# Optimization experiments

Hardware: AMD Instinct MI355X
Metric: run time of the kernel (lower is better)

The kernel has to match this reference:

```python
import jax, jax.numpy as jnp
import numpy as np

B, DIN, DOUT = 16, 64, 64
P1_, P2_, P3_ = 64, 32, 16
BN_EPS = 1e-5


def setup_inputs() -> dict:
    key = jax.random.key(0)
    ks = jax.random.split(key, 8)
    A = jax.random.normal(ks[0], (B, DIN, P1_, P2_, P3_), dtype=jnp.float32)
    ini_p = float(np.sqrt(3.0 / DOUT / DIN))
    ini_qk = float(np.sqrt(1.0 / DOUT / DIN))
    def uni(k, s):
        return jax.random.uniform(k, (DOUT, DIN), dtype=jnp.float32, minval=-s, maxval=s)
    return {
        "A": A,
        "P1": uni(ks[1], ini_p),
        "P2": uni(ks[2], ini_p),
        "P3": uni(ks[3], ini_p),
        "P4": uni(ks[4], ini_p),
        "q": uni(ks[5], ini_qk),
        "k": uni(ks[6], ini_qk),
        "gamma": jnp.ones((DOUT,), jnp.float32),
        "beta": jnp.zeros((DOUT,), jnp.float32),
        "permutation_size1": P1_,
        "permutation_size2": P2_,
        "permutation_size3": P3_,
        "BATCH_SIZE": B,
    }


def reference(A, P1, P2, P3, P4, q, k, gamma, beta,
              permutation_size1, permutation_size2, permutation_size3, BATCH_SIZE):
    b = BATCH_SIZE
    dout = P1.shape[0]
    p1, p2, p3 = permutation_size1, permutation_size2, permutation_size3
    # branch 1: full per-element channel mix  [B, dout, p1, p2, p3]
    A1 = jnp.einsum('oi,bixyz->boxyz', P1, A)
    # branch 2: mean over p3, project, broadcast over p3
    A2 = jnp.einsum('oi,bixy->boxy', P2, A.mean(-1))[..., None]
    # branch 3: mean over p2, project, broadcast over p2
    A3 = jnp.einsum('oi,bixz->boxz', P3, A.mean(-2))[:, :, :, None, :]
    # attention over p1 with flattened (p2*p3) as the contraction axis
    Q = jnp.einsum('oi,bixyz->boxyz', q, A).reshape(b, dout, p1, p2 * p3)
    K = jnp.einsum('oi,bixyz->boxyz', k, A).reshape(b, dout, p1, p2 * p3)
    Alpha = jnp.einsum('bcxm,bcym->bcxy', Q, K)  # [B, dout, p1, p1]
    Alpha_norm = jnp.abs(Alpha) / jnp.linalg.norm(Alpha, axis=3, keepdims=True)
    V = jnp.einsum('oi,bixyz->boxyz', P4, A).reshape(b, dout, p1, p2 * p3)
    Y = jnp.einsum('bcxy,bcym->bcxm', Alpha_norm, V).reshape(b, dout, p1, p2, p3)
    out = A1 + 0.1 * A2 + 0.1 * A3 + 0.1 * Y
    out = jax.nn.relu(out)
    # BatchNorm3d (training-mode batch statistics, biased variance)
    mean = out.mean(axis=(0, 2, 3, 4), keepdims=True)
    var = out.var(axis=(0, 2, 3, 4), keepdims=True)
    out = (out - mean) * jax.lax.rsqrt(var + BN_EPS)
    out = out * gamma[None, :, None, None, None] + beta[None, :, None, None, None]
    return out
```

## Files before the change

kernel.cpp:

```cpp
#include <hip/hip_runtime.h>

typedef __attribute__((ext_vector_type(8))) short short8;
typedef __attribute__((ext_vector_type(4))) float f32x4;
typedef __attribute__((ext_vector_type(8))) unsigned short u16x8;
typedef __attribute__((ext_vector_type(4))) unsigned short u16x4;
typedef __attribute__((ext_vector_type(4))) unsigned int u32x4;
typedef unsigned short u16;

#define DEVINL __device__ __forceinline__

DEVINL u16 f2bf(float f) {
  unsigned u = __builtin_bit_cast(unsigned, f);
  unsigned r = (u + 0x7fffu + ((u >> 16) & 1u)) >> 16;
  return (u16)r;
}
DEVINL float bf2f(u16 h) {
  unsigned u = ((unsigned)h) << 16;
  return __builtin_bit_cast(float, u);
}
DEVINL unsigned pk2(float a, float b) {
  return (unsigned)f2bf(a) | ((unsigned)f2bf(b) << 16);
}
DEVINL int swzc(int row, int chunk) { return chunk ^ ((row ^ (row >> 3)) & 7); }
DEVINL int tile_byte(int row, int chunk) { return row * 128 + swzc(row, chunk) * 16; }


__global__ void kw_convert(const float* __restrict__ P1, const float* __restrict__ q,
                           const float* __restrict__ k, const float* __restrict__ P4,
                           const float* __restrict__ P2, const float* __restrict__ P3,
                           u16* __restrict__ Wbf) {
  int t = threadIdx.x;
  const float* srcs[6] = {P1, q, k, P4, P2, P3};
  for (int w = 0; w < 6; ++w)
    for (int e = t; e < 4096; e += 256) Wbf[w * 4096 + e] = f2bf(srcs[w][e]);
}

__global__ __launch_bounds__(512) void k_projA(
    const float* __restrict__ A, const u16* __restrict__ Wbf, u16* __restrict__ A1,
    u16* __restrict__ Q, u16* __restrict__ Km, u16* __restrict__ V,
    float* __restrict__ A2g, float* __restrict__ m2p, int g0) {
  __shared__ __align__(16) u16 tile[256 * 64];
  __shared__ __align__(16) u16 meanT[16 * 64];
  const int t = threadIdx.x;
  const int w = t >> 6, l = t & 63;
  const int lr = l & 15, lh = l >> 4;
  const int T = blockIdx.x, bg = blockIdx.y;
  const int x = T >> 1, h = T & 1;
  const long bglob = g0 + bg;

  const int m = w & 3, sh = w >> 2;
  const u16* wb = Wbf + m * 4096;
  short8 wf[4][2];
#pragma unroll
  for (int ot = 0; ot < 4; ++ot)
#pragma unroll
    for (int ks = 0; ks < 2; ++ks)
      wf[ot][ks] = *(const short8*)(wb + (ot * 16 + lr) * 64 + ks * 32 + lh * 8);
  u16* outp = (m == 0) ? A1 : (m == 1) ? Q : (m == 2) ? Km : V;
  outp += ((long)bg * 64 + x) * 32768;
  const int odd = lh & 1;
  const int p8 = (lh >> 1) * 8;

  {
    const int s4 = t & 31, i4 = t >> 5;
    const float* ap =
        A + (bglob * 64 + i4 * 4) * 32768 + (long)x * 512 + h * 256 + s4 * 4;
#pragma unroll
    for (int si = 0; si < 2; ++si) {
      f32x4 v0 = *(const f32x4*)(ap + si * 128);
      f32x4 v1 = *(const f32x4*)(ap + si * 128 + 32768);
      f32x4 v2 = *(const f32x4*)(ap + si * 128 + 65536);
      f32x4 v3 = *(const f32x4*)(ap + si * 128 + 98304);
#pragma unroll
      for (int e = 0; e < 4; ++e) {
        int s = si * 128 + s4 * 4 + e;
        u16x4 pk = {f2bf(v0[e]), f2bf(v1[e]), f2bf(v2[e]), f2bf(v3[e])};
        *(u16x4*)((char*)tile + tile_byte(s, i4 >> 1) + (i4 & 1) * 8) = pk;
      }
    }
  }
  __syncthreads();

  {
    const int ic = t & 7, zq = (t >> 3) & 3, y16 = t >> 5;
    float acc[8] = {0, 0, 0, 0, 0, 0, 0, 0};
#pragma unroll
    for (int zz = 0; zz < 4; ++zz) {
      int row = y16 * 16 + zq * 4 + zz;
      u16x8 v = *(const u16x8*)((const char*)tile + tile_byte(row, ic));
#pragma unroll
      for (int e = 0; e < 8; ++e) acc[e] += bf2f(v[e]);
    }
#pragma unroll
    for (int e = 0; e < 8; ++e) {
      acc[e] += __shfl_xor(acc[e], 8);
      acc[e] += __shfl_xor(acc[e], 16);
    }
    if (zq == 0) {
      u16x8 pk;
#pragma unroll
      for (int e = 0; e < 8; ++e) pk[e] = f2bf(acc[e] * (1.0f / 16.0f));
      *(u16x8*)((char*)meanT + tile_byte(y16, ic)) = pk;
    }
  }
  {
    const int ic = t & 7, yg = (t >> 3) & 3, z = t >> 5;
    float acc[8] = {0, 0, 0, 0, 0, 0, 0, 0};
#pragma unroll
    for (int yy = 0; yy < 4; ++yy) {
      int row = (yg * 4 + yy) * 16 + z;
      u16x8 v = *(const u16x8*)((const char*)tile + tile_byte(row, ic));
#pragma unroll
      for (int e = 0; e < 8; ++e) acc[e] += bf2f(v[e]);
    }
#pragma unroll
    for (int e = 0; e < 8; ++e) {
      acc[e] += __shfl_xor(acc[e], 8);
      acc[e] += __shfl_xor(acc[e], 16);
    }
    if (yg == 0) {
      float* mp = m2p + (((long)bg * 64 + x) * 2 + h) * 1024 + z * 64 + ic * 8;
      *(f32x4*)(mp) = (f32x4){acc[0], acc[1], acc[2], acc[3]};
      *(f32x4*)(mp + 4) = (f32x4){acc[4], acc[5], acc[6], acc[7]};
    }
  }

  for (int stp = 0; stp < 4; ++stp) {
    const int srowE = sh * 128 + stp * 32 + lr;
    const int srowO = srowE + 16;
    short8 aE0 = *(const short8*)((const char*)tile + tile_byte(srowE, lh));
    short8 aE1 = *(const short8*)((const char*)tile + tile_byte(srowE, 4 + lh));
    short8 aO0 = *(const short8*)((const char*)tile + tile_byte(srowO, lh));
    short8 aO1 = *(const short8*)((const char*)tile + tile_byte(srowO, 4 + lh));
    const int mloc = h * 256 + sh * 128 + stp * 32 + odd * 16 + p8;
#pragma unroll
    for (int ot = 0; ot < 4; ++ot) {
      f32x4 accE = {0.0f, 0.0f, 0.0f, 0.0f}, accO = {0.0f, 0.0f, 0.0f, 0.0f};
      accE = __builtin_amdgcn_mfma_f32_16x16x32_bf16(aE0, wf[ot][0], accE, 0, 0, 0);
      accE = __builtin_amdgcn_mfma_f32_16x16x32_bf16(aE1, wf[ot][1], accE, 0, 0, 0);
      accO = __builtin_amdgcn_mfma_f32_16x16x32_bf16(aO0, wf[ot][0], accO, 0, 0, 0);
      accO = __builtin_amdgcn_mfma_f32_16x16x32_bf16(aO1, wf[ot][1], accO, 0, 0, 0);
      unsigned pE0 = pk2(accE[0], accE[1]), pE1 = pk2(accE[2], accE[3]);
      unsigned pO0 = pk2(accO[0], accO[1]), pO1 = pk2(accO[2], accO[3]);
      unsigned rE0 = __shfl_xor((int)pE0, 16), rE1 = __shfl_xor((int)pE1, 16);
      unsigned rO0 = __shfl_xor((int)pO0, 16), rO1 = __shfl_xor((int)pO1, 16);
      u32x4 sv;
      if (odd) sv = (u32x4){rO0, rO1, pO0, pO1};
      else     sv = (u32x4){pE0, pE1, rE0, rE1};
      *(u32x4*)(outp + (ot * 16 + lr) * 512 + mloc) = sv;
    }
  }
  __syncthreads();

  if (w == 0) {
    const u16* wb2 = Wbf + 4 * 4096;
    f32x4 acc2[4];
#pragma unroll
    for (int ot = 0; ot < 4; ++ot) acc2[ot] = {0.0f, 0.0f, 0.0f, 0.0f};
#pragma unroll
    for (int ks = 0; ks < 2; ++ks) {
      short8 mf = *(const short8*)((const char*)meanT + tile_byte(lr, ks * 4 + lh));
#pragma unroll
      for (int ot = 0; ot < 4; ++ot) {
        short8 w2f = *(const short8*)(wb2 + (ot * 16 + lr) * 64 + ks * 32 + lh * 8);
        acc2[ot] = __builtin_amdgcn_mfma_f32_16x16x32_bf16(w2f, mf, acc2[ot], 0, 0, 0);
      }
    }
#pragma unroll
    for (int ot = 0; ot < 4; ++ot)
#pragma unroll
      for (int r = 0; r < 4; ++r) {
        int o = ot * 16 + lh * 4 + r;
        A2g[(((long)bg * 64 + o) * 64 + x) * 32 + h * 16 + lr] = acc2[ot][r];
      }
  }
}

__global__ __launch_bounds__(256) void k_a3fin(const float* __restrict__ m2p,
                                               const float* __restrict__ P3,
                                               float* __restrict__ A3g, int g0) {
  __shared__ float m2s[16 * 65];
  const int t = threadIdx.x;
  const int x = blockIdx.x, bg = blockIdx.y;
  const float* mp = m2p + ((long)bg * 64 + x) * 2048;
  {
    int e = t * 4;
    int z = e >> 6, i = e & 63;
    f32x4 v0 = *(const f32x4*)(mp + e);
    f32x4 v1 = *(const f32x4*)(mp + 1024 + e);
#pragma unroll
    for (int j = 0; j < 4; ++j) m2s[z * 65 + i + j] = (v0[j] + v1[j]) * (1.0f / 32.0f);
  }
  __syncthreads();
  const int z = t & 15, og = t >> 4;
#pragma unroll
  for (int oo = 0; oo < 4; ++oo) {
    int o = og * 4 + oo;
    float acc = 0.0f;
#pragma unroll 8
    for (int i = 0; i < 64; ++i) acc += P3[o * 64 + i] * m2s[z * 65 + i];
    A3g[(((long)bg * 64 + o) * 64 + x) * 16 + z] = acc;
  }
}

__global__ __launch_bounds__(256) void k_attn(const u16* __restrict__ Qg,
                                              const u16* __restrict__ Kg,
                                              const u16* __restrict__ Vg,
                                              const u16* __restrict__ A1g,
                                              const float* __restrict__ A2g,
                                              const float* __restrict__ A3g,
                                              u16* __restrict__ outbf,
                                              float* __restrict__ partials, int g0) {
  __shared__ __align__(16) u16 Qc[4096], Kc[4096];
  __shared__ __align__(16) u16 Vt[2][4096];
  __shared__ __align__(16) u16 An[4096];
  __shared__ float red[8];
  const int t = threadIdx.x, w = t >> 6, l = t & 63;
  const int lr = l & 15, lh = l >> 4;
  const int c = blockIdx.x, bg = blockIdx.y;
  const long bglob = g0 + bg;
  const long base = (long)bg * 2097152 + (long)c * 512;
  const u16* Qp = Qg + base;
  const u16* Kp = Kg + base;
  const u16* Vp = Vg + base;
  const u16* A1p = A1g + base;

  const int m4 = t & 15, y4 = t >> 4;
  const int odd = lh & 1;
  const int p8 = (lh >> 1) * 8;

  u16x4 vr[4];
#pragma unroll
  for (int r = 0; r < 4; ++r)
    vr[r] = *(const u16x4*)(Vp + (long)(y4 * 4 + r) * 32768 + m4 * 4);

  f32x4 accA[4];
#pragma unroll
  for (int yt = 0; yt < 4; ++yt) accA[yt] = {0.0f, 0.0f, 0.0f, 0.0f};

  const int srow = t >> 3, scc = t & 7;
  u16x8 qpre[2], kpre[2];
#pragma unroll
  for (int it = 0; it < 2; ++it) {
    int row = srow + it * 32;
    int gch = scc ^ ((row ^ (row >> 3)) & 7);
    qpre[it] = *(const u16x8*)(Qp + (long)row * 32768 + gch * 8);
    kpre[it] = *(const u16x8*)(Kp + (long)row * 32768 + gch * 8);
  }
  for (int mc = 0; mc < 8; ++mc) {
#pragma unroll
    for (int it = 0; it < 2; ++it) {
      int row = srow + it * 32;
      *(u16x8*)((char*)Qc + row * 128 + scc * 16) = qpre[it];
      *(u16x8*)((char*)Kc + row * 128 + scc * 16) = kpre[it];
    }
    asm volatile("s_waitcnt lgkmcnt(0)" ::: "memory");
    __builtin_amdgcn_s_barrier();
    __builtin_amdgcn_sched_barrier(0);
    if (mc < 7) {
      const int nc = (mc + 1) * 64;
#pragma unroll
      for (int it = 0; it < 2; ++it) {
        int row = srow + it * 32;
        int gch = scc ^ ((row ^ (row >> 3)) & 7);
        qpre[it] = *(const u16x8*)(Qp + (long)row * 32768 + nc + gch * 8);
        kpre[it] = *(const u16x8*)(Kp + (long)row * 32768 + nc + gch * 8);
      }
    }
    short8 qf[2];
#pragma unroll
    for (int ks = 0; ks < 2; ++ks)
      qf[ks] = *(const short8*)((const char*)Qc + tile_byte(16 * w + lr, ks * 4 + lh));
#pragma unroll
    for (int ks = 0; ks < 2; ++ks)
#pragma unroll
      for (int yt = 0; yt < 4; ++yt) {
        short8 kf = *(const short8*)((const char*)Kc + tile_byte(yt * 16 + lr, ks * 4 + lh));
        accA[yt] = __builtin_amdgcn_mfma_f32_16x16x32_bf16(qf[ks], kf, accA[yt], 0, 0, 0);
      }
    asm volatile("s_waitcnt lgkmcnt(0)" ::: "memory");
    __builtin_amdgcn_s_barrier();
    __builtin_amdgcn_sched_barrier(0);
  }

  float rsq[4];
#pragma unroll
  for (int r = 0; r < 4; ++r) {
    float s = 0.0f;
#pragma unroll
    for (int yt = 0; yt < 4; ++yt) s += accA[yt][r] * accA[yt][r];
#pragma unroll
    for (int msk = 1; msk < 16; msk <<= 1) s += __shfl_xor(s, msk);
    rsq[r] = rsqrtf(s);
  }
#pragma unroll
  for (int yt = 0; yt < 4; ++yt)
#pragma unroll
    for (int r = 0; r < 4; ++r) {
      int xr = 16 * w + 4 * lh + r;
      int y = yt * 16 + lr;
      *(u16*)((char*)An + xr * 128 + swzc(xr, y >> 3) * 16 + (y & 7) * 2) =
          f2bf(fabsf(accA[yt][r]) * rsq[r]);
    }

  float ls = 0.0f, lsq = 0.0f;
  const float* A2p = A2g + ((long)bg * 64 + c) * 2048;
  const float* A3p = A3g + ((long)bg * 64 + c) * 1024;
  u16* outp = outbf + (long)bglob * 2097152 + (long)c * 512;
  const int x = 16 * w + lr;
  const f32x4 a3lo = *(const f32x4*)(A3p + x * 16 + p8);
  const f32x4 a3hi = *(const f32x4*)(A3p + x * 16 + p8 + 4);

  for (int mc = 0; mc < 8; ++mc) {
    u16* vbuf = Vt[mc & 1];
#pragma unroll
    for (int ci = 0; ci < 4; ++ci) {
      int mrow = m4 * 4 + ci;
      u16x4 pk = {vr[0][ci], vr[1][ci], vr[2][ci], vr[3][ci]};
      *(u16x4*)((char*)vbuf + tile_byte(mrow, y4 >> 1) + (y4 & 1) * 8) = pk;
    }
    asm volatile("s_waitcnt lgkmcnt(0)" ::: "memory");
    __builtin_amdgcn_s_barrier();
    __builtin_amdgcn_sched_barrier(0);
    if (mc < 7) {
      const int nc = (mc + 1) * 64;
#pragma unroll
      for (int r = 0; r < 4; ++r)
        vr[r] = *(const u16x4*)(Vp + (long)(y4 * 4 + r) * 32768 + nc + m4 * 4);
    }

    f32x4 accY[4];
#pragma unroll
    for (int mt = 0; mt < 4; ++mt) accY[mt] = {0.0f, 0.0f, 0.0f, 0.0f};
#pragma unroll
    for (int ks = 0; ks < 2; ++ks) {
      short8 anf = *(const short8*)((const char*)An + tile_byte(16 * w + lr, ks * 4 + lh));
#pragma unroll
      for (int mt = 0; mt < 4; ++mt) {
        short8 vf = *(const short8*)((const char*)vbuf + tile_byte(mt * 16 + lr, ks * 4 + lh));
        accY[mt] = __builtin_amdgcn_mfma_f32_16x16x32_bf16(vf, anf, accY[mt], 0, 0, 0);
      }
    }
#pragma unroll
    for (int pair = 0; pair < 2; ++pair) {
      f32x4 aE = accY[2 * pair], aO = accY[2 * pair + 1];
      f32x4 rE, rO;
#pragma unroll
      for (int j = 0; j < 4; ++j) {
        rE[j] = __shfl_xor(aE[j], 16);
        rO[j] = __shfl_xor(aO[j], 16);
      }
      const int mb = mc * 64 + pair * 32 + odd * 16 + p8;
      const float a2v = A2p[x * 32 + (mb >> 4)];
      u16x8 a1v = *(const u16x8*)(A1p + (long)x * 32768 + mb);
      u16x8 o;
#pragma unroll
      for (int r = 0; r < 8; ++r) {
        float yv = (r < 4) ? (odd ? rO[r] : aE[r]) : (odd ? aO[r - 4] : rE[r - 4]);
        float a3v = (r < 4) ? a3lo[r] : a3hi[r - 4];
        float val = bf2f(a1v[r]) + 0.1f * (a2v + a3v + yv);
        val = fmaxf(val, 0.0f);
        o[r] = f2bf(val);
        ls += val;
        lsq += val * val;
      }
      *(u16x8*)(outp + (long)x * 32768 + mb) = o;
    }
  }

#pragma unroll
  for (int off = 32; off > 0; off >>= 1) {
    ls += __shfl_xor(ls, off);
    lsq += __shfl_xor(lsq, off);
  }
  if (l == 0) {
    red[w] = ls;
    red[4 + w] = lsq;
  }
  __syncthreads();
  if (t == 0) {
    partials[2 * (bglob * 64 + c) + 0] = red[0] + red[1] + red[2] + red[3];
    partials[2 * (bglob * 64 + c) + 1] = red[4] + red[5] + red[6] + red[7];
  }
}

__global__ void k_stats(const float* __restrict__ partials, const float* __restrict__ gamma,
                        const float* __restrict__ beta, float* __restrict__ sb) {
  int c = threadIdx.x;
  if (c >= 64) return;
  float S = 0.0f, SQ = 0.0f;
  for (int b = 0; b < 16; ++b) {
    S += partials[2 * (b * 64 + c) + 0];
    SQ += partials[2 * (b * 64 + c) + 1];
  }
  const float N = 524288.0f;
  float mean = S / N;
  float var = SQ / N - mean * mean;
  float rs = rsqrtf(var + 1e-5f);
  float scale = gamma[c] * rs;
  sb[c] = scale;
  sb[64 + c] = beta[c] - mean * scale;
}

__global__ __launch_bounds__(256) void k_bn(const u16* __restrict__ outbf,
                                            float* __restrict__ out,
                                            const float* __restrict__ sb) {
  const int x = blockIdx.x & 63, b = blockIdx.x >> 6;
  const u16* tin = outbf + ((long)b * 64 + x) * 32768;
  float* outb = out + (long)b * 2097152 + (long)x * 512;
#pragma unroll
  for (int rep = 0; rep < 16; ++rep) {
    int e = rep * 2048 + threadIdx.x * 8;
    int cc = e >> 9, mm = e & 511;
    u16x8 v = *(const u16x8*)(tin + e);
    float scale = sb[cc], bias = sb[64 + cc];
    f32x4 o0, o1;
#pragma unroll
    for (int r = 0; r < 4; ++r) {
      o0[r] = bf2f(v[r]) * scale + bias;
      o1[r] = bf2f(v[4 + r]) * scale + bias;
    }
    float* op = outb + (long)cc * 32768 + mm;
    *(f32x4*)(op) = o0;
    *(f32x4*)(op + 4) = o1;
  }
}

extern "C" void kernel_launch(void* const* d_in, const int* in_sizes, int n_in, void* d_out,
                              int out_size, void* d_ws, size_t ws_size, hipStream_t stream) {
  (void)in_sizes; (void)n_in; (void)out_size;
  const float* A = (const float*)d_in[0];
  const float* P1 = (const float*)d_in[1];
  const float* P2 = (const float*)d_in[2];
  const float* P3 = (const float*)d_in[3];
  const float* P4 = (const float*)d_in[4];
  const float* q = (const float*)d_in[5];
  const float* k = (const float*)d_in[6];
  const float* gamma = (const float*)d_in[7];
  const float* beta = (const float*)d_in[8];
  float* out = (float*)d_out;
  char* ws = (char*)d_ws;

  u16* Wbf = (u16*)ws;
  float* partials = (float*)(ws + 49152);
  float* sb = (float*)(ws + 57344);
  const size_t GR = 65536;
  const size_t OUTBF = (size_t)16 * 64 * 32768 * 2;
  u16* outbf = (u16*)(ws + GR);
  const size_t SZ_M = (size_t)64 * 32768 * 2;
  const size_t SZ_A2 = (size_t)64 * 64 * 32 * 4;
  const size_t SZ_A3 = (size_t)64 * 64 * 16 * 4;
  const size_t SZ_M2 = (size_t)64 * 2 * 16 * 64 * 4;
  const size_t perb = 4 * SZ_M + SZ_A2 + SZ_A3 + SZ_M2;
  const size_t base0 = GR + OUTBF;
  int G = 1;
  if (ws_size > base0 + perb) G = (int)((ws_size - base0) / perb);
  if (G > 8) G = 8;
  if (G < 1) G = 1;

  u16* A1 = (u16*)(ws + base0);
  u16* Qw = (u16*)(ws + base0 + (size_t)G * SZ_M);
  u16* Kw = (u16*)(ws + base0 + (size_t)G * SZ_M * 2);
  u16* Vw = (u16*)(ws + base0 + (size_t)G * SZ_M * 3);
  float* A2 = (float*)(ws + base0 + (size_t)G * SZ_M * 4);
  float* A3 = (float*)((char*)A2 + (size_t)G * SZ_A2);
  float* m2p = (float*)((char*)A3 + (size_t)G * SZ_A3);

  kw_convert<<<1, 256, 0, stream>>>(P1, q, k, P4, P2, P3, Wbf);
  for (int g0 = 0; g0 < 16; g0 += G) {
    int Gc = (16 - g0) < G ? (16 - g0) : G;
    k_projA<<<dim3(128, Gc), 512, 0, stream>>>(A, Wbf, A1, Qw, Kw, Vw, A2, m2p, g0);
    k_a3fin<<<dim3(64, Gc), 256, 0, stream>>>(m2p, P3, A3, g0);
    k_attn<<<dim3(64, Gc), 256, 0, stream>>>(Qw, Kw, Vw, A1, A2, A3, outbf, partials, g0);
  }
  k_stats<<<1, 64, 0, stream>>>(partials, gamma, beta, sb);
  k_bn<<<1024, 256, 0, stream>>>(outbf, out, sb);
}
```

Before: 247.1 us.

## Split attention blocks over query-row halves to double grid parallelism

```diff
diff --git a/kernel.cpp b/kernel.cpp
--- a/kernel.cpp
+++ b/kernel.cpp
@@ -211,13 +211,16 @@
                                               const float* __restrict__ A3g,
                                               u16* __restrict__ outbf,
                                               float* __restrict__ partials, int g0) {
-  __shared__ __align__(16) u16 Qc[4096], Kc[4096];
+  __shared__ __align__(16) u16 Qc[2048];
+  __shared__ __align__(16) u16 Kc[4096];
   __shared__ __align__(16) u16 Vt[2][4096];
-  __shared__ __align__(16) u16 An[4096];
+  __shared__ __align__(16) u16 An[2048];
+  __shared__ float red2[4][64][4];
   __shared__ float red[8];
   const int t = threadIdx.x, w = t >> 6, l = t & 63;
   const int lr = l & 15, lh = l >> 4;
-  const int c = blockIdx.x, bg = blockIdx.y;
+  const int bx = blockIdx.x, bg = blockIdx.y;
+  const int c = bx & 63, xh = bx >> 6;
   const long bglob = g0 + bg;
   const long base = (long)bg * 2097152 + (long)c * 512;
   const u16* Qp = Qg + base;
@@ -225,6 +228,9 @@
   const u16* Vp = Vg + base;
   const u16* A1p = A1g + base;
 
+  const int wx = w >> 1, wy = w & 1;
+  const int xloc = wx * 16 + lr;
+  const int xg = xh * 32 + xloc;
   const int m4 = t & 15, y4 = t >> 4;
   const int odd = lh & 1;
   const int p8 = (lh >> 1) * 8;
@@ -234,24 +240,25 @@
   for (int r = 0; r < 4; ++r)
     vr[r] = *(const u16x4*)(Vp + (long)(y4 * 4 + r) * 32768 + m4 * 4);
 
-  f32x4 accA[4];
-#pragma unroll
-  for (int yt = 0; yt < 4; ++yt) accA[yt] = {0.0f, 0.0f, 0.0f, 0.0f};
+  f32x4 accA[2];
+#pragma unroll
+  for (int yt = 0; yt < 2; ++yt) accA[yt] = {0.0f, 0.0f, 0.0f, 0.0f};
 
   const int srow = t >> 3, scc = t & 7;
-  u16x8 qpre[2], kpre[2];
+  const int gchq = scc ^ ((srow ^ (srow >> 3)) & 7);
+  u16x8 qpre, kpre[2];
+  qpre = *(const u16x8*)(Qp + (long)(xh * 32 + srow) * 32768 + gchq * 8);
 #pragma unroll
   for (int it = 0; it < 2; ++it) {
     int row = srow + it * 32;
     int gch = scc ^ ((row ^ (row >> 3)) & 7);
-    qpre[it] = *(const u16x8*)(Qp + (long)row * 32768 + gch * 8);
     kpre[it] = *(const u16x8*)(Kp + (long)row * 32768 + gch * 8);
   }
   for (int mc = 0; mc < 8; ++mc) {
+    *(u16x8*)((char*)Qc + srow * 128 + scc * 16) = qpre;
 #pragma unroll
     for (int it = 0; it < 2; ++it) {
       int row = srow + it * 32;
-      *(u16x8*)((char*)Qc + row * 128 + scc * 16) = qpre[it];
       *(u16x8*)((char*)Kc + row * 128 + scc * 16) = kpre[it];
     }
     asm volatile("s_waitcnt lgkmcnt(0)" ::: "memory");
@@ -259,23 +266,24 @@
     __builtin_amdgcn_sched_barrier(0);
     if (mc < 7) {
       const int nc = (mc + 1) * 64;
+      qpre = *(const u16x8*)(Qp + (long)(xh * 32 + srow) * 32768 + nc + gchq * 8);
 #pragma unroll
       for (int it = 0; it < 2; ++it) {
         int row = srow + it * 32;
         int gch = scc ^ ((row ^ (row >> 3)) & 7);
-        qpre[it] = *(const u16x8*)(Qp + (long)row * 32768 + nc + gch * 8);
         kpre[it] = *(const u16x8*)(Kp + (long)row * 32768 + nc + gch * 8);
       }
     }
     short8 qf[2];
 #pragma unroll
     for (int ks = 0; ks < 2; ++ks)
-      qf[ks] = *(const short8*)((const char*)Qc + tile_byte(16 * w + lr, ks * 4 + lh));
+      qf[ks] = *(const short8*)((const char*)Qc + tile_byte(xloc, ks * 4 + lh));
 #pragma unroll
     for (int ks = 0; ks < 2; ++ks)
 #pragma unroll
-      for (int yt = 0; yt < 4; ++yt) {
-        short8 kf = *(const short8*)((const char*)Kc + tile_byte(yt * 16 + lr, ks * 4 + lh));
+      for (int yt = 0; yt < 2; ++yt) {
+        int yrow = (wy * 2 + yt) * 16 + lr;
+        short8 kf = *(const short8*)((const char*)Kc + tile_byte(yrow, ks * 4 + lh));
         accA[yt] = __builtin_amdgcn_mfma_f32_16x16x32_bf16(qf[ks], kf, accA[yt], 0, 0, 0);
       }
     asm volatile("s_waitcnt lgkmcnt(0)" ::: "memory");
@@ -283,22 +291,25 @@
     __builtin_amdgcn_sched_barrier(0);
   }
 
+  float spart[4];
+#pragma unroll
+  for (int r = 0; r < 4; ++r) {
+    float s = accA[0][r] * accA[0][r] + accA[1][r] * accA[1][r];
+#pragma unroll
+    for (int msk = 1; msk < 16; msk <<= 1) s += __shfl_xor(s, msk);
+    spart[r] = s;
+    red2[w][l][r] = s;
+  }
+  __syncthreads();
   float rsq[4];
 #pragma unroll
-  for (int r = 0; r < 4; ++r) {
-    float s = 0.0f;
-#pragma unroll
-    for (int yt = 0; yt < 4; ++yt) s += accA[yt][r] * accA[yt][r];
-#pragma unroll
-    for (int msk = 1; msk < 16; msk <<= 1) s += __shfl_xor(s, msk);
-    rsq[r] = rsqrtf(s);
-  }
-#pragma unroll
-  for (int yt = 0; yt < 4; ++yt)
+  for (int r = 0; r < 4; ++r) rsq[r] = rsqrtf(spart[r] + red2[w ^ 1][l][r]);
+#pragma unroll
+  for (int yt = 0; yt < 2; ++yt)
 #pragma unroll
     for (int r = 0; r < 4; ++r) {
-      int xr = 16 * w + 4 * lh + r;
-      int y = yt * 16 + lr;
+      int xr = wx * 16 + 4 * lh + r;
+      int y = (wy * 2 + yt) * 16 + lr;
       *(u16*)((char*)An + xr * 128 + swzc(xr, y >> 3) * 16 + (y & 7) * 2) =
           f2bf(fabsf(accA[yt][r]) * rsq[r]);
     }
@@ -307,9 +318,8 @@
   const float* A2p = A2g + ((long)bg * 64 + c) * 2048;
   const float* A3p = A3g + ((long)bg * 64 + c) * 1024;
   u16* outp = outbf + (long)bglob * 2097152 + (long)c * 512;
-  const int x = 16 * w + lr;
-  const f32x4 a3lo = *(const f32x4*)(A3p + x * 16 + p8);
-  const f32x4 a3hi = *(const f32x4*)(A3p + x * 16 + p8 + 4);
+  const f32x4 a3lo = *(const f32x4*)(A3p + xg * 16 + p8);
+  const f32x4 a3hi = *(const f32x4*)(A3p + xg * 16 + p8 + 4);
 
   for (int mc = 0; mc < 8; ++mc) {
     u16* vbuf = Vt[mc & 1];
@@ -329,30 +339,30 @@
         vr[r] = *(const u16x4*)(Vp + (long)(y4 * 4 + r) * 32768 + nc + m4 * 4);
     }
 
-    f32x4 accY[4];
-#pragma unroll
-    for (int mt = 0; mt < 4; ++mt) accY[mt] = {0.0f, 0.0f, 0.0f, 0.0f};
+    f32x4 accY[2];
+#pragma unroll
+    for (int mt2 = 0; mt2 < 2; ++mt2) accY[mt2] = {0.0f, 0.0f, 0.0f, 0.0f};
 #pragma unroll
     for (int ks = 0; ks < 2; ++ks) {
-      short8 anf = *(const short8*)((const char*)An + tile_byte(16 * w + lr, ks * 4 + lh));
-#pragma unroll
-      for (int mt = 0; mt < 4; ++mt) {
+      short8 anf = *(const short8*)((const char*)An + tile_byte(xloc, ks * 4 + lh));
+#pragma unroll
+      for (int mt2 = 0; mt2 < 2; ++mt2) {
+        int mt = wy * 2 + mt2;
         short8 vf = *(const short8*)((const char*)vbuf + tile_byte(mt * 16 + lr, ks * 4 + lh));
-        accY[mt] = __builtin_amdgcn_mfma_f32_16x16x32_bf16(vf, anf, accY[mt], 0, 0, 0);
-      }
-    }
-#pragma unroll
-    for (int pair = 0; pair < 2; ++pair) {
-      f32x4 aE = accY[2 * pair], aO = accY[2 * pair + 1];
+        accY[mt2] = __builtin_amdgcn_mfma_f32_16x16x32_bf16(vf, anf, accY[mt2], 0, 0, 0);
+      }
+    }
+    {
+      f32x4 aE = accY[0], aO = accY[1];
       f32x4 rE, rO;
 #pragma unroll
       for (int j = 0; j < 4; ++j) {
         rE[j] = __shfl_xor(aE[j], 16);
         rO[j] = __shfl_xor(aO[j], 16);
       }
-      const int mb = mc * 64 + pair * 32 + odd * 16 + p8;
-      const float a2v = A2p[x * 32 + (mb >> 4)];
-      u16x8 a1v = *(const u16x8*)(A1p + (long)x * 32768 + mb);
+      const int mb = mc * 64 + wy * 32 + odd * 16 + p8;
+      const float a2v = A2p[xg * 32 + (mb >> 4)];
+      u16x8 a1v = *(const u16x8*)(A1p + (long)xg * 32768 + mb);
       u16x8 o;
 #pragma unroll
       for (int r = 0; r < 8; ++r) {
@@ -364,7 +374,7 @@
         ls += val;
         lsq += val * val;
       }
-      *(u16x8*)(outp + (long)x * 32768 + mb) = o;
+      *(u16x8*)(outp + (long)xg * 32768 + mb) = o;
     }
   }
 
@@ -379,8 +389,9 @@
   }
   __syncthreads();
   if (t == 0) {
-    partials[2 * (bglob * 64 + c) + 0] = red[0] + red[1] + red[2] + red[3];
-    partials[2 * (bglob * 64 + c) + 1] = red[4] + red[5] + red[6] + red[7];
+    long pi = ((bglob * 64 + c) * 2 + xh) * 2;
+    partials[pi + 0] = red[0] + red[1] + red[2] + red[3];
+    partials[pi + 1] = red[4] + red[5] + red[6] + red[7];
   }
 }
 
@@ -389,10 +400,12 @@
   int c = threadIdx.x;
   if (c >= 64) return;
   float S = 0.0f, SQ = 0.0f;
-  for (int b = 0; b < 16; ++b) {
-    S += partials[2 * (b * 64 + c) + 0];
-    SQ += partials[2 * (b * 64 + c) + 1];
-  }
+  for (int b = 0; b < 16; ++b)
+    for (int xh = 0; xh < 2; ++xh) {
+      long pi = (((long)b * 64 + c) * 2 + xh) * 2;
+      S += partials[pi + 0];
+      SQ += partials[pi + 1];
+    }
   const float N = 524288.0f;
   float mean = S / N;
   float var = SQ / N - mean * mean;
@@ -443,8 +456,8 @@
 
   u16* Wbf = (u16*)ws;
   float* partials = (float*)(ws + 49152);
-  float* sb = (float*)(ws + 57344);
-  const size_t GR = 65536;
+  float* sb = (float*)(ws + 65536);
+  const size_t GR = 98304;
   const size_t OUTBF = (size_t)16 * 64 * 32768 * 2;
   u16* outbf = (u16*)(ws + GR);
   const size_t SZ_M = (size_t)64 * 32768 * 2;
@@ -471,7 +484,7 @@
     int Gc = (16 - g0) < G ? (16 - g0) : G;
     k_projA<<<dim3(128, Gc), 512, 0, stream>>>(A, Wbf, A1, Qw, Kw, Vw, A2, m2p, g0);
     k_a3fin<<<dim3(64, Gc), 256, 0, stream>>>(m2p, P3, A3, g0);
-    k_attn<<<dim3(64, Gc), 256, 0, stream>>>(Qw, Kw, Vw, A1, A2, A3, outbf, partials, g0);
+    k_attn<<<dim3(128, Gc), 256, 0, stream>>>(Qw, Kw, Vw, A1, A2, A3, outbf, partials, g0);
   }
   k_stats<<<1, 64, 0, stream>>>(partials, gamma, beta, sb);
   k_bn<<<1024, 256, 0, stream>>>(outbf, out, sb);
```

New measurement: 247.8 us. Within noise of the previous version (+0.3%).
